# Kernel optimization log

Measured on AMD Instinct MI355X. Metric: run time of the kernel, lower is better.

## Reference

```python
import jax, jax.numpy as jnp
import numpy as np

EMBED_DIM = 1024
NUM_HEADS = 16
HEAD_DIM = EMBED_DIM // NUM_HEADS


def setup_inputs() -> dict:
    key = jax.random.key(0)
    ks = jax.random.split(key, 10)
    s = 1.0 / np.sqrt(EMBED_DIM)
    x = jax.random.normal(ks[0], (4, 2048, EMBED_DIM), dtype=jnp.float32)
    return {
        "x": x,
        "Wq": jax.random.normal(ks[1], (EMBED_DIM, EMBED_DIM), jnp.float32) * s,
        "bq": jnp.zeros((EMBED_DIM,), jnp.float32),
        "Wk": jax.random.normal(ks[2], (EMBED_DIM, EMBED_DIM), jnp.float32) * s,
        "bk": jnp.zeros((EMBED_DIM,), jnp.float32),
        "Wv": jax.random.normal(ks[3], (EMBED_DIM, EMBED_DIM), jnp.float32) * s,
        "bv": jnp.zeros((EMBED_DIM,), jnp.float32),
        "Wo": jax.random.normal(ks[4], (EMBED_DIM, EMBED_DIM), jnp.float32) * s,
        "bo": jnp.zeros((EMBED_DIM,), jnp.float32),
        "head_scaling": jnp.ones((NUM_HEADS,), jnp.float32),
    }


def reference(x, Wq, bq, Wk, bk, Wv, bv, Wo, bo, head_scaling):
    B, S, E = x.shape
    H, D = NUM_HEADS, HEAD_DIM
    scale = 1.0 / np.sqrt(D)
    # projections (torch Linear: y = x @ W.T + b)
    q = (x @ Wq.T + bq).reshape(B, S, H, D).transpose(0, 2, 1, 3)  # [B,H,S,D]
    k = (x @ Wk.T + bk).reshape(B, S, H, D).transpose(0, 2, 1, 3)
    v = (x @ Wv.T + bv).reshape(B, S, H, D).transpose(0, 2, 1, 3)
    scores = jnp.einsum("bhqd,bhkd->bhqk", q, k) * scale
    attn = jax.nn.softmax(scores, axis=-1)
    head_imp = jax.nn.softmax(head_scaling)[None, :, None, None]  # [1,H,1,1]
    attn = attn * head_imp
    out = jnp.einsum("bhqk,bhkd->bhqd", attn, v)
    out = out.transpose(0, 2, 1, 3).reshape(B, S, E)
    return out @ Wo.T + bo
```

## Files before the change

kernel.cpp:

```cpp
#include <hip/hip_runtime.h>

typedef __bf16 bf16x8 __attribute__((ext_vector_type(8)));
typedef float f32x4 __attribute__((ext_vector_type(4)));

constexpr int E = 1024;
constexpr int T = 8192;
constexpr size_t TE  = (size_t)T * E;
constexpr size_t WSZ = (size_t)E * E;

#define QSCALE 0.18033688011112042f

__device__ __forceinline__ unsigned short f2bf(float f) {
    union { float f; unsigned int i; } x; x.f = f;
    unsigned int i = x.i;
    return (unsigned short)((i + 0x7fffu + ((i >> 16) & 1u)) >> 16);
}

__device__ __forceinline__ unsigned int pack_rtz(float lo, float hi) {
    return __builtin_amdgcn_perm(
        __builtin_bit_cast(unsigned int, hi),
        __builtin_bit_cast(unsigned int, lo), 0x07060302u);
}

__device__ __forceinline__ void gload16(const unsigned short* g, unsigned short* l) {
    __builtin_amdgcn_global_load_lds(
        (const __attribute__((address_space(1))) unsigned int*)g,
        (__attribute__((address_space(3))) unsigned int*)l, 16, 0, 0);
}

__global__ __launch_bounds__(256)
void cvt_kernel(const float* __restrict__ x,
                const float* __restrict__ w0, const float* __restrict__ w1,
                const float* __restrict__ w2, const float* __restrict__ w3,
                unsigned short* __restrict__ xb, unsigned short* __restrict__ wb)
{
    size_t i = ((size_t)blockIdx.x * 256 + threadIdx.x) * 8;
    const float* src;
    unsigned short* dst;
    if (i < TE) { src = x + i; dst = xb + i; }
    else {
        size_t j = i - TE;
        int w = (int)(j >> 20);
        size_t off = j & (WSZ - 1);
        src = (w == 0 ? w0 : w == 1 ? w1 : w == 2 ? w2 : w3) + off;
        dst = wb + ((size_t)w << 20) + off;
    }
    float4 a = *(const float4*)src;
    float4 b = *(const float4*)(src + 4);
    union { unsigned short u[8]; uint4 v; } p;
    p.u[0] = f2bf(a.x); p.u[1] = f2bf(a.y); p.u[2] = f2bf(a.z); p.u[3] = f2bf(a.w);
    p.u[4] = f2bf(b.x); p.u[5] = f2bf(b.y); p.u[6] = f2bf(b.z); p.u[7] = f2bf(b.w);
    *(uint4*)dst = p.v;
}

template <int MODE>
__device__ __forceinline__ void gemm_body(const unsigned short* __restrict__ X,
                                          const unsigned short* __restrict__ W,
                                          const float* __restrict__ bias,
                                          void* __restrict__ outp, int t0, int n0,
                                          float oscale)
{
    __shared__ unsigned short As[128 * 32];
    __shared__ unsigned short Bs[128 * 32];

    const int tid  = threadIdx.x;
    const int wave = tid >> 6;
    const int lane = tid & 63;
    const int quad = lane >> 4;
    const int l16  = lane & 15;
    const int wm   = wave >> 1;
    const int wn   = wave & 1;
    const int ldr  = lane >> 2;
    const int ldc  = (lane & 3) ^ ((lane >> 3) & 3);
    const int fsw  = (l16 >> 1) & 3;

    f32x4 acc[4][4];
#pragma unroll
    for (int i = 0; i < 4; i++)
#pragma unroll
        for (int j = 0; j < 4; j++)
            acc[i][j] = (f32x4){0.f, 0.f, 0.f, 0.f};

    for (int k0 = 0; k0 < E; k0 += 32) {
#pragma unroll
        for (int n = 0; n < 2; n++) {
            const int row = wave * 32 + n * 16;
            gload16(&X[(size_t)(t0 + row + ldr) * E + k0 + ldc * 8], &As[row * 32 + lane * 8]);
            gload16(&W[(size_t)(n0 + row + ldr) * E + k0 + ldc * 8], &Bs[row * 32 + lane * 8]);
        }
        __syncthreads();

        bf16x8 af[4], bfr[4];
#pragma unroll
        for (int i = 0; i < 4; i++)
            af[i] = *(const bf16x8*)&As[(wm * 64 + i * 16 + l16) * 32 + (quad ^ fsw) * 8];
#pragma unroll
        for (int j = 0; j < 4; j++)
            bfr[j] = *(const bf16x8*)&Bs[(wn * 64 + j * 16 + l16) * 32 + (quad ^ fsw) * 8];

#pragma unroll
        for (int i = 0; i < 4; i++)
#pragma unroll
            for (int j = 0; j < 4; j++) {
                if (MODE == 2)
                    acc[i][j] = __builtin_amdgcn_mfma_f32_16x16x32_bf16(af[i], bfr[j], acc[i][j], 0, 0, 0);
                else
                    acc[i][j] = __builtin_amdgcn_mfma_f32_16x16x32_bf16(bfr[j], af[i], acc[i][j], 0, 0, 0);
            }
        __syncthreads();
    }

    if (MODE == 2) {
#pragma unroll
        for (int j = 0; j < 4; j++) {
            const int gc = n0 + wn * 64 + j * 16 + l16;
            const float bj = bias[gc];
#pragma unroll
            for (int i = 0; i < 4; i++) {
                const int gr0 = t0 + wm * 64 + i * 16 + quad * 4;
                union { unsigned short u[4]; uint2 v; } o;
#pragma unroll
                for (int r = 0; r < 4; r++) o.u[r] = f2bf((acc[i][j][r] + bj) * oscale);
                unsigned short* vt = (unsigned short*)outp;
                *(uint2*)&vt[((size_t)((gr0 >> 11) * 16 + (gc >> 6)) * 64 + (gc & 63)) * 2048 + (gr0 & 2047)] = o.v;
            }
        }
    } else {
#pragma unroll
        for (int j = 0; j < 4; j++) {
            const int nb = n0 + wn * 64 + j * 16 + quad * 4;
            const float4 b4 = *(const float4*)&bias[nb];
#pragma unroll
            for (int i = 0; i < 4; i++) {
                const int t = t0 + wm * 64 + i * 16 + l16;
                if (MODE == 1) {
                    float4 o;
                    o.x = (acc[i][j][0] + b4.x) * oscale;
                    o.y = (acc[i][j][1] + b4.y) * oscale;
                    o.z = (acc[i][j][2] + b4.z) * oscale;
                    o.w = (acc[i][j][3] + b4.w) * oscale;
                    *(float4*)&((float*)outp)[(size_t)t * E + nb] = o;
                } else {
                    union { unsigned short u[4]; uint2 v; } o;
                    o.u[0] = f2bf((acc[i][j][0] + b4.x) * oscale);
                    o.u[1] = f2bf((acc[i][j][1] + b4.y) * oscale);
                    o.u[2] = f2bf((acc[i][j][2] + b4.z) * oscale);
                    o.u[3] = f2bf((acc[i][j][3] + b4.w) * oscale);
                    *(uint2*)&((unsigned short*)outp)[(size_t)t * E + nb] = o.v;
                }
            }
        }
    }
}

__global__ __launch_bounds__(256)
void gemm_qkv(const unsigned short* __restrict__ Xb, const unsigned short* __restrict__ Wb,
              const float* __restrict__ bq, const float* __restrict__ bk, const float* __restrict__ bv,
              unsigned short* __restrict__ Qb, unsigned short* __restrict__ Kb, unsigned short* __restrict__ VTb)
{
    const int t0 = blockIdx.x * 128;
    const int y = blockIdx.y;
    const int seg = y >> 3;
    const int n0 = (y & 7) * 128;
    const unsigned short* W = Wb + (size_t)seg * WSZ;
    if (seg == 0)      gemm_body<0>(Xb, W, bq, Qb,  t0, n0, QSCALE);
    else if (seg == 1) gemm_body<0>(Xb, W, bk, Kb,  t0, n0, 1.0f);
    else               gemm_body<2>(Xb, W, bv, VTb, t0, n0, 1.0f);
}

__global__ __launch_bounds__(256)
void gemm_out(const unsigned short* __restrict__ AOb, const unsigned short* __restrict__ Wob,
              const float* __restrict__ bo, float* __restrict__ out)
{
    gemm_body<1>(AOb, Wob, bo, out, blockIdx.x * 128, blockIdx.y * 128, 1.0f);
}

__global__ __launch_bounds__(256, 4)
void attn_kernel(const unsigned short* __restrict__ Q,
                 const unsigned short* __restrict__ K,
                 const unsigned short* __restrict__ VT,
                 const float* __restrict__ hs,
                 unsigned short* __restrict__ AO)
{
    constexpr int S = 2048, H = 16;
    const int hb = blockIdx.x;
    const int qt = blockIdx.y;
    const int h  = hb >> 2;
    const int b  = hb & 3;

    const int tid  = threadIdx.x;
    const int wave = tid >> 6;
    const int lane = tid & 63;
    const int quad = lane >> 4;
    const int l16  = lane & 15;

    __shared__ unsigned short Kpl[2][2 * 32 * 32];
    __shared__ unsigned short Vpl[2][64 * 32];

    float mx = -1e30f;
    for (int i = 0; i < H; i++) mx = fmaxf(mx, hs[i]);
    float ss = 0.f;
    for (int i = 0; i < H; i++) ss += __expf(hs[i] - mx);
    const float head_imp = __expf(hs[h] - mx) / ss;

    const int base_t  = b * S;
    const int colbase = h * 64;
    const int q0 = qt * 128 + wave * 32;

    bf16x8 qf[2][2];
#pragma unroll
    for (int qi = 0; qi < 2; qi++)
#pragma unroll
        for (int c = 0; c < 2; c++)
            qf[qi][c] = *(const bf16x8*)&Q[(size_t)(base_t + q0 + qi * 16 + l16) * E + colbase + c * 32 + quad * 8];

    f32x4 oT[2][4];
#pragma unroll
    for (int qi = 0; qi < 2; qi++)
#pragma unroll
        for (int t = 0; t < 4; t++) oT[qi][t] = (f32x4){0.f, 0.f, 0.f, 0.f};
    f32x4 l4[2];
    l4[0] = (f32x4){0.f, 0.f, 0.f, 0.f};
    l4[1] = (f32x4){0.f, 0.f, 0.f, 0.f};

    const int sc   = (lane & 3) ^ ((lane >> 3) & 3);
    const int krow = (tid >> 2) & 31;
    const int kch  = tid >> 7;
    const int vrow = tid >> 2;
    const int fsw  = (l16 >> 1) & 3;
    const unsigned short* const vbase = VT + (size_t)(b * 16 + h) * 64 * 2048;

    auto stage = [&](int kt, int bu) {
        const int kbase = base_t + kt * 32;
        gload16(&K[(size_t)(kbase + krow) * E + colbase + kch * 32 + sc * 8], &Kpl[bu][tid * 8]);
        gload16(&vbase[(size_t)vrow * 2048 + kt * 32 + sc * 8], &Vpl[bu][tid * 8]);
    };

    stage(0, 0);

    for (int kt = 0; kt < 64; kt++) {
        __syncthreads();
        if (kt < 63) stage(kt + 1, (kt + 1) & 1);
        const int cb = kt & 1;

        bf16x8 kf[2][2];
#pragma unroll
        for (int tk = 0; tk < 2; tk++)
#pragma unroll
            for (int ch = 0; ch < 2; ch++)
                kf[tk][ch] = *(const bf16x8*)&Kpl[cb][ch * 1024 + (tk * 16 + l16) * 32 + (quad ^ fsw) * 8];

        unsigned int pbw[2][4];
#pragma unroll
        for (int qi = 0; qi < 2; qi++) {
            unsigned int pw[4];
#pragma unroll
            for (int tk = 0; tk < 2; tk++) {
                f32x4 st = (f32x4){0.f, 0.f, 0.f, 0.f};
                st = __builtin_amdgcn_mfma_f32_16x16x32_bf16(kf[tk][0], qf[qi][0], st, 0, 0, 0);
                st = __builtin_amdgcn_mfma_f32_16x16x32_bf16(kf[tk][1], qf[qi][1], st, 0, 0, 0);
                float p0 = __builtin_amdgcn_exp2f(st[0]);
                float p1 = __builtin_amdgcn_exp2f(st[1]);
                float p2 = __builtin_amdgcn_exp2f(st[2]);
                float p3 = __builtin_amdgcn_exp2f(st[3]);
                l4[qi][0] += p0; l4[qi][1] += p1; l4[qi][2] += p2; l4[qi][3] += p3;
                pw[tk * 2 + 0] = pack_rtz(p0, p1);
                pw[tk * 2 + 1] = pack_rtz(p2, p3);
            }
            auto s1 = __builtin_amdgcn_permlane32_swap(pw[0], pw[2], false, false);
            auto s2 = __builtin_amdgcn_permlane32_swap(pw[1], pw[3], false, false);
            auto t1 = __builtin_amdgcn_permlane16_swap(s1[0], s1[1], false, false);
            auto t2 = __builtin_amdgcn_permlane16_swap(s2[0], s2[1], false, false);
            pbw[qi][0] = t1[0];
            pbw[qi][1] = t2[0];
            pbw[qi][2] = t1[1];
            pbw[qi][3] = t2[1];
        }

#pragma unroll
        for (int tau = 0; tau < 4; tau++) {
            bf16x8 vf = *(const bf16x8*)&Vpl[cb][(tau * 16 + l16) * 32 + (quad ^ fsw) * 8];
#pragma unroll
            for (int qi = 0; qi < 2; qi++) {
                union { unsigned int w[4]; bf16x8 v; } pb;
                pb.w[0] = pbw[qi][0]; pb.w[1] = pbw[qi][1];
                pb.w[2] = pbw[qi][2]; pb.w[3] = pbw[qi][3];
                oT[qi][tau] = __builtin_amdgcn_mfma_f32_16x16x32_bf16(vf, pb.v, oT[qi][tau], 0, 0, 0);
            }
        }
    }

#pragma unroll
    for (int qi = 0; qi < 2; qi++) {
        float l = l4[qi][0] + l4[qi][1] + l4[qi][2] + l4[qi][3];
        l += __shfl_xor(l, 16);
        l += __shfl_xor(l, 32);
        const float inv = head_imp / l;
#pragma unroll
        for (int tau = 0; tau < 4; tau++) {
            union { unsigned short u[4]; uint2 v; } o;
#pragma unroll
            for (int r = 0; r < 4; r++) o.u[r] = f2bf(oT[qi][tau][r] * inv);
            *(uint2*)&AO[(size_t)(base_t + q0 + qi * 16 + l16) * E + colbase + tau * 16 + quad * 4] = o.v;
        }
    }
}

extern "C" void kernel_launch(void* const* d_in, const int* in_sizes, int n_in,
                              void* d_out, int out_size, void* d_ws, size_t ws_size,
                              hipStream_t stream)
{
    const float* x  = (const float*)d_in[0];
    const float* Wq = (const float*)d_in[1];
    const float* bq = (const float*)d_in[2];
    const float* Wk = (const float*)d_in[3];
    const float* bk = (const float*)d_in[4];
    const float* Wv = (const float*)d_in[5];
    const float* bv = (const float*)d_in[6];
    const float* Wo = (const float*)d_in[7];
    const float* bo = (const float*)d_in[8];
    const float* hs = (const float*)d_in[9];
    float* out = (float*)d_out;

    unsigned short* ws = (unsigned short*)d_ws;
    unsigned short* xb  = ws;
    unsigned short* wb  = ws + TE;
    unsigned short* Qb  = ws + TE + 4 * WSZ;
    unsigned short* AOb = Qb + TE;
    unsigned short* Kb  = (unsigned short*)d_out;
    unsigned short* VTb = Kb + TE;

    dim3 bb(256, 1, 1);
    hipLaunchKernelGGL(cvt_kernel, dim3(6144, 1, 1), bb, 0, stream, x, Wq, Wk, Wv, Wo, xb, wb);
    hipLaunchKernelGGL(gemm_qkv, dim3(64, 24, 1), bb, 0, stream, xb, wb, bq, bk, bv, Qb, Kb, VTb);
    hipLaunchKernelGGL(attn_kernel, dim3(64, 16, 1), bb, 0, stream, Qb, Kb, VTb, hs, AOb);
    hipLaunchKernelGGL(gemm_out, dim3(64, 8, 1), bb, 0, stream, AOb, wb + 3 * WSZ, bo, out);
}
```

Before: 282.8 us.

## Compute softmax row sums via MFMA with ones vector, add setprio and pointer increments

Replaces the per-element VALU accumulation of softmax denominators with an extra MFMA against a ones fragment, so the sum is taken from the bf16-rounded probabilities that feed the PV product. It also switches staging to incrementing global pointers, unrolls the KV loop by 2, and raises wave priority around the PV MFMA block. The goal is to cut VALU work and address arithmetic in the inner loop, at the cost of extra MFMA issue slots and a cross-lane shuffle at the end.

```diff
diff --git a/kernel.cpp b/kernel.cpp
--- a/kernel.cpp
+++ b/kernel.cpp
@@ -214,14 +214,21 @@
         for (int c = 0; c < 2; c++)
             qf[qi][c] = *(const bf16x8*)&Q[(size_t)(base_t + q0 + qi * 16 + l16) * E + colbase + c * 32 + quad * 8];
 
+    union { unsigned short u[8]; bf16x8 v; } onesf;
+    {
+        const unsigned short ov = (l16 == 0) ? (unsigned short)0x3F80 : (unsigned short)0;
+#pragma unroll
+        for (int j = 0; j < 8; j++) onesf.u[j] = ov;
+    }
+
     f32x4 oT[2][4];
 #pragma unroll
     for (int qi = 0; qi < 2; qi++)
 #pragma unroll
         for (int t = 0; t < 4; t++) oT[qi][t] = (f32x4){0.f, 0.f, 0.f, 0.f};
-    f32x4 l4[2];
-    l4[0] = (f32x4){0.f, 0.f, 0.f, 0.f};
-    l4[1] = (f32x4){0.f, 0.f, 0.f, 0.f};
+    f32x4 oT5[2];
+    oT5[0] = (f32x4){0.f, 0.f, 0.f, 0.f};
+    oT5[1] = (f32x4){0.f, 0.f, 0.f, 0.f};
 
     const int sc   = (lane & 3) ^ ((lane >> 3) & 3);
     const int krow = (tid >> 2) & 31;
@@ -230,17 +237,22 @@
     const int fsw  = (l16 >> 1) & 3;
     const unsigned short* const vbase = VT + (size_t)(b * 16 + h) * 64 * 2048;
 
-    auto stage = [&](int kt, int bu) {
-        const int kbase = base_t + kt * 32;
-        gload16(&K[(size_t)(kbase + krow) * E + colbase + kch * 32 + sc * 8], &Kpl[bu][tid * 8]);
-        gload16(&vbase[(size_t)vrow * 2048 + kt * 32 + sc * 8], &Vpl[bu][tid * 8]);
+    const unsigned short* kg = &K[(size_t)(base_t + krow) * E + colbase + kch * 32 + sc * 8];
+    const unsigned short* vg = &vbase[(size_t)vrow * 2048 + sc * 8];
+
+    auto stage = [&](int bu) {
+        gload16(kg, &Kpl[bu][tid * 8]);
+        gload16(vg, &Vpl[bu][tid * 8]);
+        kg += 32 * E;
+        vg += 32;
     };
 
-    stage(0, 0);
-
+    stage(0);
+
+#pragma unroll 2
     for (int kt = 0; kt < 64; kt++) {
         __syncthreads();
-        if (kt < 63) stage(kt + 1, (kt + 1) & 1);
+        if (kt < 63) stage((kt + 1) & 1);
         const int cb = kt & 1;
 
         bf16x8 kf[2][2];
@@ -250,7 +262,7 @@
             for (int ch = 0; ch < 2; ch++)
                 kf[tk][ch] = *(const bf16x8*)&Kpl[cb][ch * 1024 + (tk * 16 + l16) * 32 + (quad ^ fsw) * 8];
 
-        unsigned int pbw[2][4];
+        union { unsigned int w[4]; bf16x8 v; } pb[2];
 #pragma unroll
         for (int qi = 0; qi < 2; qi++) {
             unsigned int pw[4];
@@ -263,7 +275,6 @@
                 float p1 = __builtin_amdgcn_exp2f(st[1]);
                 float p2 = __builtin_amdgcn_exp2f(st[2]);
                 float p3 = __builtin_amdgcn_exp2f(st[3]);
-                l4[qi][0] += p0; l4[qi][1] += p1; l4[qi][2] += p2; l4[qi][3] += p3;
                 pw[tk * 2 + 0] = pack_rtz(p0, p1);
                 pw[tk * 2 + 1] = pack_rtz(p2, p3);
             }
@@ -271,30 +282,29 @@
             auto s2 = __builtin_amdgcn_permlane32_swap(pw[1], pw[3], false, false);
             auto t1 = __builtin_amdgcn_permlane16_swap(s1[0], s1[1], false, false);
             auto t2 = __builtin_amdgcn_permlane16_swap(s2[0], s2[1], false, false);
-            pbw[qi][0] = t1[0];
-            pbw[qi][1] = t2[0];
-            pbw[qi][2] = t1[1];
-            pbw[qi][3] = t2[1];
-        }
-
+            pb[qi].w[0] = t1[0];
+            pb[qi].w[1] = t2[0];
+            pb[qi].w[2] = t1[1];
+            pb[qi].w[3] = t2[1];
+        }
+
+        __builtin_amdgcn_s_setprio(1);
 #pragma unroll
         for (int tau = 0; tau < 4; tau++) {
             bf16x8 vf = *(const bf16x8*)&Vpl[cb][(tau * 16 + l16) * 32 + (quad ^ fsw) * 8];
 #pragma unroll
-            for (int qi = 0; qi < 2; qi++) {
-                union { unsigned int w[4]; bf16x8 v; } pb;
-                pb.w[0] = pbw[qi][0]; pb.w[1] = pbw[qi][1];
-                pb.w[2] = pbw[qi][2]; pb.w[3] = pbw[qi][3];
-                oT[qi][tau] = __builtin_amdgcn_mfma_f32_16x16x32_bf16(vf, pb.v, oT[qi][tau], 0, 0, 0);
-            }
-        }
+            for (int qi = 0; qi < 2; qi++)
+                oT[qi][tau] = __builtin_amdgcn_mfma_f32_16x16x32_bf16(vf, pb[qi].v, oT[qi][tau], 0, 0, 0);
+        }
+#pragma unroll
+        for (int qi = 0; qi < 2; qi++)
+            oT5[qi] = __builtin_amdgcn_mfma_f32_16x16x32_bf16(onesf.v, pb[qi].v, oT5[qi], 0, 0, 0);
+        __builtin_amdgcn_s_setprio(0);
     }
 
 #pragma unroll
     for (int qi = 0; qi < 2; qi++) {
-        float l = l4[qi][0] + l4[qi][1] + l4[qi][2] + l4[qi][3];
-        l += __shfl_xor(l, 16);
-        l += __shfl_xor(l, 32);
+        const float l = __shfl(oT5[qi][0], l16);
         const float inv = head_imp / l;
 #pragma unroll
         for (int tau = 0; tau < 4; tau++) {
```

Measured after the change: 274.6 us. 2.9% less time.
